# Kernel tuning notes

Measured on AMD Instinct MI355X. Metric: run time of the kernel, lower is better.

The kernel has to match this reference:

```python
import jax, jax.numpy as jnp
import numpy as np

WINDOW = 3
PAD = WINDOW // 2
NUM_PATTERNS = 10000


def setup_inputs() -> dict:
    key = jax.random.key(0)
    k1, k2, k3, k4 = jax.random.split(key, 4)
    B, C, H, W = 4, 32, 512, 512
    E, OUT = 64, 64
    x = jax.random.normal(k1, (B, C, H, W), dtype=jnp.float32)
    table = jax.random.normal(k2, (NUM_PATTERNS, E), dtype=jnp.float32)
    proj_w = jax.random.normal(k3, (OUT, E), dtype=jnp.float32) * 0.1
    proj_b = jax.random.normal(k4, (OUT,), dtype=jnp.float32) * 0.1
    return {"x": x, "table": table, "proj_w": proj_w, "proj_b": proj_b}


def reference(x, table, proj_w, proj_b):
    # x: (B, C, H, W)
    B, C, H, W = x.shape
    P = table.shape[0]
    # replicate padding (torch F.pad mode='replicate')
    xp = jnp.pad(x, ((0, 0), (0, 0), (PAD, PAD), (PAD, PAD)), mode='edge')
    # quantize once per pixel; torch (.long()) truncates toward zero
    q = jnp.trunc(xp * 100.0).astype(jnp.int32)  # (B, C, H+2, W+2)
    h = jnp.zeros((B, C, H, W), dtype=jnp.int32)
    for di in range(WINDOW):
        for dj in range(WINDOW):
            h = h + q[:, :, di:di + H, dj:dj + W]
    idx_c = jnp.abs(h) % P                      # (B, C, H, W), nonneg
    # indices.float().mean(dim=1).long(): mean over channels then truncate
    idx = jnp.mean(idx_c.astype(jnp.float32), axis=1).astype(jnp.int32)  # (B, H, W)
    emb = table[idx]                             # (B, H, W, E) gather
    out = emb @ proj_w.T + proj_b                # (B, H, W, OUT)
    return jnp.transpose(out, (0, 3, 1, 2))      # (B, OUT, H, W)
```

## Files before the change

kernel.cpp:

```cpp
#include <hip/hip_runtime.h>


#define CH  32
#define HH  512
#define WW  512
#define EE  64
#define OUT 64
#define PP  10000

#define TWPX 128
#define HW   (HH * WW)

typedef float f32x4 __attribute__((ext_vector_type(4)));

__global__ __launch_bounds__(256) void proj_kernel(
    const float* __restrict__ table, const float* __restrict__ pw,
    const float* __restrict__ pb, float* __restrict__ tpT) {
  __shared__ float sW[EE * OUT];
  const int t = threadIdx.x;
  for (int i = t; i < EE * OUT; i += 256) {
    int o = i >> 6, e = i & 63;
    sW[e * OUT + o] = pw[i];
  }
  __syncthreads();
  const int o  = t & 63;
  const int pr = t >> 6;
  const int p0 = blockIdx.x * 16 + pr;
  const float4* r0 = (const float4*)(table + (size_t)(p0     ) * EE);
  const float4* r1 = (const float4*)(table + (size_t)(p0 +  4) * EE);
  const float4* r2 = (const float4*)(table + (size_t)(p0 +  8) * EE);
  const float4* r3 = (const float4*)(table + (size_t)(p0 + 12) * EE);
  float a0 = pb[o], a1 = pb[o], a2 = pb[o], a3 = pb[o];
  float b0 = 0.f,  b1 = 0.f,  b2 = 0.f,  b3 = 0.f;
  #pragma unroll
  for (int e4 = 0; e4 < EE / 4; ++e4) {
    float4 t0 = r0[e4], t1 = r1[e4], t2 = r2[e4], t3 = r3[e4];
    float w0 = sW[(4 * e4 + 0) * OUT + o];
    float w1 = sW[(4 * e4 + 1) * OUT + o];
    float w2 = sW[(4 * e4 + 2) * OUT + o];
    float w3 = sW[(4 * e4 + 3) * OUT + o];
    a0 = fmaf(t0.x, w0, a0); b0 = fmaf(t0.y, w1, b0);
    a0 = fmaf(t0.z, w2, a0); b0 = fmaf(t0.w, w3, b0);
    a1 = fmaf(t1.x, w0, a1); b1 = fmaf(t1.y, w1, b1);
    a1 = fmaf(t1.z, w2, a1); b1 = fmaf(t1.w, w3, b1);
    a2 = fmaf(t2.x, w0, a2); b2 = fmaf(t2.y, w1, b2);
    a2 = fmaf(t2.z, w2, a2); b2 = fmaf(t2.w, w3, b2);
    a3 = fmaf(t3.x, w0, a3); b3 = fmaf(t3.y, w1, b3);
    a3 = fmaf(t3.z, w2, a3); b3 = fmaf(t3.w, w3, b3);
  }
  float* oc = tpT + (size_t)o * PP;
  oc[p0]      = a0 + b0;
  oc[p0 + 4]  = a1 + b1;
  oc[p0 + 8]  = a2 + b2;
  oc[p0 + 12] = a3 + b3;
}

__device__ __forceinline__ int q3(float a, float b, float c) {
  return (int)(a * 100.0f) + (int)(b * 100.0f) + (int)(c * 100.0f);
}

__global__ __launch_bounds__(256) void idx_kernel(
    const float* __restrict__ x, unsigned short* __restrict__ idx16) {
  const int tx  = threadIdx.x;
  const int ty  = threadIdx.y;
  const int gx0 = blockIdx.x * TWPX;
  const int y   = blockIdx.y * 4 + ty;
  const int b   = blockIdx.z;
  const int x0  = gx0 + tx * 2;

  const int ym1 = max(y - 1, 0);
  const int yp1 = min(y + 1, HH - 1);
  const size_t rm1 = (size_t)ym1 * WW + x0;
  const size_t r0  = (size_t)y   * WW + x0;
  const size_t rp1 = (size_t)yp1 * WW + x0;

  const bool edge = (tx == 0) || (tx == 63);
  const int  ecol = (tx == 0) ? max(gx0 - 1, 0) : min(gx0 + TWPX, WW - 1);
  const size_t em1 = (size_t)ym1 * WW + ecol;
  const size_t e0  = (size_t)y   * WW + ecol;
  const size_t ep1 = (size_t)yp1 * WW + ecol;

  const float* xb = x + (size_t)b * CH * HW;

  int acc0 = 0, acc1 = 0;
  #pragma unroll 2
  for (int c = 0; c < CH; ++c) {
    const float* xc = xb + (size_t)c * HW;
    float2 a = *(const float2*)(xc + rm1);
    float2 m = *(const float2*)(xc + r0);
    float2 p = *(const float2*)(xc + rp1);

    int cs0 = q3(a.x, m.x, p.x);
    int cs1 = q3(a.y, m.y, p.y);

    int csl = __shfl(cs1, tx - 1, 64);
    int csr = __shfl(cs0, tx + 1, 64);
    if (edge) {
      int e = q3(xc[em1], xc[e0], xc[ep1]);
      if (tx == 0) csl = e; else csr = e;
    }

    int h0 = csl + cs0 + cs1;
    int h1 = cs0 + cs1 + csr;

    acc0 += (int)((unsigned)(h0 < 0 ? -h0 : h0) % PP);
    acc1 += (int)((unsigned)(h1 < 0 ? -h1 : h1) % PP);
  }
  const unsigned i0 = (unsigned)(acc0 >> 5), i1 = (unsigned)(acc1 >> 5);

  const size_t pix = (size_t)b * HW + (size_t)y * WW + x0;
  *(unsigned*)(idx16 + pix) = i0 | (i1 << 16);
}

__global__ __launch_bounds__(256) void expand3_kernel(
    const unsigned short* __restrict__ idx16, const float* __restrict__ tpT,
    float* __restrict__ out) {
  const int t = threadIdx.x;
  const unsigned bid   = blockIdx.x;
  const int      chunk = bid & 31;
  const int      o     = (bid >> 5) & 63;
  const int      b     = bid >> 11;

  const float* col = tpT + (size_t)o * PP;
  const size_t pixbase = (size_t)chunk * 8192;
  const unsigned short* ip = idx16 + (size_t)b * HW + pixbase;
  float* op = out + ((size_t)b * OUT + o) * HW + pixbase;

  uint2 pk0 = *(const uint2*)(ip + 0 * 1024 + t * 4);
  uint2 pk1 = *(const uint2*)(ip + 1 * 1024 + t * 4);
  uint2 pk2 = *(const uint2*)(ip + 2 * 1024 + t * 4);
  uint2 pk3 = *(const uint2*)(ip + 3 * 1024 + t * 4);
  uint2 pk4 = *(const uint2*)(ip + 4 * 1024 + t * 4);
  uint2 pk5 = *(const uint2*)(ip + 5 * 1024 + t * 4);
  uint2 pk6 = *(const uint2*)(ip + 6 * 1024 + t * 4);
  uint2 pk7 = *(const uint2*)(ip + 7 * 1024 + t * 4);

#define EXPAND_ONE(pk, j)                                                  \
  {                                                                        \
    const unsigned i0 = pk.x & 0xFFFFu, i1 = pk.x >> 16;                   \
    const unsigned i2 = pk.y & 0xFFFFu, i3 = pk.y >> 16;                   \
    f32x4 v = { col[i0], col[i1], col[i2], col[i3] };                      \
    __builtin_nontemporal_store(v, (f32x4*)(op + (j) * 1024 + t * 4));     \
  }

  EXPAND_ONE(pk0, 0)
  EXPAND_ONE(pk1, 1)
  EXPAND_ONE(pk2, 2)
  EXPAND_ONE(pk3, 3)
  EXPAND_ONE(pk4, 4)
  EXPAND_ONE(pk5, 5)
  EXPAND_ONE(pk6, 6)
  EXPAND_ONE(pk7, 7)
#undef EXPAND_ONE
}

extern "C" void kernel_launch(void* const* d_in, const int* in_sizes, int n_in,
                              void* d_out, int out_size, void* d_ws, size_t ws_size,
                              hipStream_t stream) {
  const float* x     = (const float*)d_in[0];
  const float* table = (const float*)d_in[1];
  const float* pw    = (const float*)d_in[2];
  const float* pb    = (const float*)d_in[3];
  float* out = (float*)d_out;

  const int B = in_sizes[0] / (CH * HW);

  float* tpT = (float*)d_ws;
  unsigned short* idx16 =
      (unsigned short*)((char*)d_ws + (size_t)OUT * PP * 4);

  proj_kernel<<<PP / 16, 256, 0, stream>>>(table, pw, pb, tpT);

  dim3 block(64, 4, 1);
  dim3 grid(WW / TWPX, HH / 4, B);
  idx_kernel<<<grid, block, 0, stream>>>(x, idx16);

  const int nblk = B * OUT * 32;
  expand3_kernel<<<nblk, 256, 0, stream>>>(idx16, tpT, out);
}
```

Measured before the change: 116.4 us.

## Compute two output rows per wave with full-row tiles in idx kernel

```diff
diff --git a/kernel.cpp b/kernel.cpp
--- a/kernel.cpp
+++ b/kernel.cpp
@@ -8,7 +8,6 @@
 #define OUT 64
 #define PP  10000
 
-#define TWPX 128
 #define HW   (HH * WW)
 
 typedef float f32x4 __attribute__((ext_vector_type(4)));
@@ -55,61 +54,94 @@
   oc[p0 + 12] = a3 + b3;
 }
 
-__device__ __forceinline__ int q3(float a, float b, float c) {
-  return (int)(a * 100.0f) + (int)(b * 100.0f) + (int)(c * 100.0f);
-}
-
-__global__ __launch_bounds__(256) void idx_kernel(
+__device__ __forceinline__ int qv(float v) { return (int)(v * 100.0f); }
+
+__device__ __forceinline__ int modp(int h) {
+  return (int)((unsigned)(h < 0 ? -h : h) % PP);
+}
+
+__global__ __launch_bounds__(128) void idx_kernel(
     const float* __restrict__ x, unsigned short* __restrict__ idx16) {
-  const int tx  = threadIdx.x;
-  const int ty  = threadIdx.y;
-  const int gx0 = blockIdx.x * TWPX;
-  const int y   = blockIdx.y * 4 + ty;
-  const int b   = blockIdx.z;
-  const int x0  = gx0 + tx * 2;
-
-  const int ym1 = max(y - 1, 0);
-  const int yp1 = min(y + 1, HH - 1);
-  const size_t rm1 = (size_t)ym1 * WW + x0;
-  const size_t r0  = (size_t)y   * WW + x0;
-  const size_t rp1 = (size_t)yp1 * WW + x0;
-
-  const bool edge = (tx == 0) || (tx == 63);
-  const int  ecol = (tx == 0) ? max(gx0 - 1, 0) : min(gx0 + TWPX, WW - 1);
-  const size_t em1 = (size_t)ym1 * WW + ecol;
-  const size_t e0  = (size_t)y   * WW + ecol;
-  const size_t ep1 = (size_t)yp1 * WW + ecol;
+  const int t    = threadIdx.x;
+  const int lane = t & 63;
+  const int w    = t >> 6;
+  const int b    = blockIdx.y;
+  const int ya   = blockIdx.x * 4 + 2 * w;
+  const int x0   = lane * 8;
+
+  const int ru = max(ya - 1, 0);
+  const int rd = min(ya + 2, HH - 1);
+  const size_t o0 = (size_t)ru * WW + x0;
+  const size_t o1 = (size_t)ya * WW + x0;
+  const size_t o2 = (size_t)(ya + 1) * WW + x0;
+  const size_t o3 = (size_t)rd * WW + x0;
 
   const float* xb = x + (size_t)b * CH * HW;
 
-  int acc0 = 0, acc1 = 0;
+  int accA[8], accB[8];
+  #pragma unroll
+  for (int j = 0; j < 8; ++j) { accA[j] = 0; accB[j] = 0; }
+
   #pragma unroll 2
   for (int c = 0; c < CH; ++c) {
     const float* xc = xb + (size_t)c * HW;
-    float2 a = *(const float2*)(xc + rm1);
-    float2 m = *(const float2*)(xc + r0);
-    float2 p = *(const float2*)(xc + rp1);
-
-    int cs0 = q3(a.x, m.x, p.x);
-    int cs1 = q3(a.y, m.y, p.y);
-
-    int csl = __shfl(cs1, tx - 1, 64);
-    int csr = __shfl(cs0, tx + 1, 64);
-    if (edge) {
-      int e = q3(xc[em1], xc[e0], xc[ep1]);
-      if (tx == 0) csl = e; else csr = e;
+    float4 a0 = *(const float4*)(xc + o0);
+    float4 a1 = *(const float4*)(xc + o0 + 4);
+    float4 b0 = *(const float4*)(xc + o1);
+    float4 b1 = *(const float4*)(xc + o1 + 4);
+    float4 c0 = *(const float4*)(xc + o2);
+    float4 c1 = *(const float4*)(xc + o2 + 4);
+    float4 d0 = *(const float4*)(xc + o3);
+    float4 d1 = *(const float4*)(xc + o3 + 4);
+
+    int q0[8] = { qv(a0.x), qv(a0.y), qv(a0.z), qv(a0.w),
+                  qv(a1.x), qv(a1.y), qv(a1.z), qv(a1.w) };
+    int q1[8] = { qv(b0.x), qv(b0.y), qv(b0.z), qv(b0.w),
+                  qv(b1.x), qv(b1.y), qv(b1.z), qv(b1.w) };
+    int q2[8] = { qv(c0.x), qv(c0.y), qv(c0.z), qv(c0.w),
+                  qv(c1.x), qv(c1.y), qv(c1.z), qv(c1.w) };
+    int q3[8] = { qv(d0.x), qv(d0.y), qv(d0.z), qv(d0.w),
+                  qv(d1.x), qv(d1.y), qv(d1.z), qv(d1.w) };
+
+    int csA[8], csB[8];
+    #pragma unroll
+    for (int j = 0; j < 8; ++j) {
+      int m = q1[j] + q2[j];
+      csA[j] = q0[j] + m;
+      csB[j] = m + q3[j];
     }
 
-    int h0 = csl + cs0 + cs1;
-    int h1 = cs0 + cs1 + csr;
-
-    acc0 += (int)((unsigned)(h0 < 0 ? -h0 : h0) % PP);
-    acc1 += (int)((unsigned)(h1 < 0 ? -h1 : h1) % PP);
-  }
-  const unsigned i0 = (unsigned)(acc0 >> 5), i1 = (unsigned)(acc1 >> 5);
-
-  const size_t pix = (size_t)b * HW + (size_t)y * WW + x0;
-  *(unsigned*)(idx16 + pix) = i0 | (i1 << 16);
+    int Al = __shfl(csA[7], (lane - 1) & 63, 64);
+    int Ar = __shfl(csA[0], (lane + 1) & 63, 64);
+    int Bl = __shfl(csB[7], (lane - 1) & 63, 64);
+    int Br = __shfl(csB[0], (lane + 1) & 63, 64);
+    if (lane == 0)  { Al = csA[0]; Bl = csB[0]; }
+    if (lane == 63) { Ar = csA[7]; Br = csB[7]; }
+
+    accA[0] += modp(Al + csA[0] + csA[1]);
+    accB[0] += modp(Bl + csB[0] + csB[1]);
+    #pragma unroll
+    for (int j = 1; j < 7; ++j) {
+      accA[j] += modp(csA[j - 1] + csA[j] + csA[j + 1]);
+      accB[j] += modp(csB[j - 1] + csB[j] + csB[j + 1]);
+    }
+    accA[7] += modp(csA[6] + csA[7] + Ar);
+    accB[7] += modp(csB[6] + csB[7] + Br);
+  }
+
+  uint4 pa, pb_;
+  pa.x  = (unsigned)(accA[0] >> 5) | ((unsigned)(accA[1] >> 5) << 16);
+  pa.y  = (unsigned)(accA[2] >> 5) | ((unsigned)(accA[3] >> 5) << 16);
+  pa.z  = (unsigned)(accA[4] >> 5) | ((unsigned)(accA[5] >> 5) << 16);
+  pa.w  = (unsigned)(accA[6] >> 5) | ((unsigned)(accA[7] >> 5) << 16);
+  pb_.x = (unsigned)(accB[0] >> 5) | ((unsigned)(accB[1] >> 5) << 16);
+  pb_.y = (unsigned)(accB[2] >> 5) | ((unsigned)(accB[3] >> 5) << 16);
+  pb_.z = (unsigned)(accB[4] >> 5) | ((unsigned)(accB[5] >> 5) << 16);
+  pb_.w = (unsigned)(accB[6] >> 5) | ((unsigned)(accB[7] >> 5) << 16);
+
+  unsigned short* orow = idx16 + (size_t)b * HW + (size_t)ya * WW + x0;
+  *(uint4*)(orow)      = pa;
+  *(uint4*)(orow + WW) = pb_;
 }
 
 __global__ __launch_bounds__(256) void expand3_kernel(
@@ -171,9 +203,8 @@
 
   proj_kernel<<<PP / 16, 256, 0, stream>>>(table, pw, pb, tpT);
 
-  dim3 block(64, 4, 1);
-  dim3 grid(WW / TWPX, HH / 4, B);
-  idx_kernel<<<grid, block, 0, stream>>>(x, idx16);
+  dim3 grid(HH / 4, B);
+  idx_kernel<<<grid, 128, 0, stream>>>(x, idx16);
 
   const int nblk = B * OUT * 32;
   expand3_kernel<<<nblk, 256, 0, stream>>>(idx16, tpT, out);
```

Measured after the change: 110.9 us. 1.05x faster.
